# Kernel optimization log

Hardware: AMD Instinct MI355X
Metric: run time of the kernel (lower is better)

Reference implementation:

```python
import jax, jax.numpy as jnp
import numpy as np

D_INPUT = 2048
DD_DIM = 512
DD_PAIRS = DD_DIM // 2


def setup_inputs() -> dict:
    key = jax.random.key(0)
    k1, k2, k3 = jax.random.split(key, 3)
    x = jax.random.normal(k1, (4, 4096, D_INPUT), dtype=jnp.float32)
    # Learned projection (zeros at init in torch; use small random for a non-trivial test)
    W = jax.random.normal(k2, (DD_PAIRS, D_INPUT), dtype=jnp.float32) * 0.02
    b = jax.random.normal(k3, (DD_PAIRS,), dtype=jnp.float32) * 0.02
    return {"x": x, "W": W, "b": b}


def reference(x, W, b):
    # x: (B, T, D); W: (P, D); b: (P,) with P = DD_DIM // 2
    deltas = jnp.einsum('btd,pd->btp', x, W) + b          # (B, T, P)
    angles = jnp.cumsum(deltas, axis=1)                   # cumulative phase
    cos, sin = jnp.cos(angles), jnp.sin(angles)
    x1 = x[..., :DD_PAIRS]                                # (B, T, P)
    x2 = x[..., DD_PAIRS:DD_DIM]                          # (B, T, P)
    rotated = jnp.concatenate([x1 * cos - x2 * sin, x2 * cos + x1 * sin], axis=-1)
    return jnp.concatenate([rotated, x[..., DD_DIM:]], axis=-1)
```

## Files before the change

### kernel.cpp

```cpp
#include <hip/hip_runtime.h>
#include <math.h>

#define BB 4
#define TT 4096
#define DDIM 2048
#define PP 256
#define MM (BB*TT)
#define KKDIM 2048
#define CHUNK 32
#define NCHUNK (TT/CHUNK)

#define BK 64
#define KSTEPS (KKDIM/BK)
#define LSTRA 72

typedef __attribute__((ext_vector_type(8))) short short8;
typedef __attribute__((ext_vector_type(4))) float f32x4;

__device__ __forceinline__ unsigned short f2bf(float f) {
    unsigned u = __float_as_uint(f);
    u += 0x7FFF + ((u >> 16) & 1);
    return (unsigned short)(u >> 16);
}
__device__ __forceinline__ float bf2f(unsigned short h) {
    return __uint_as_float(((unsigned)h) << 16);
}

__device__ __forceinline__ void cvt8(const float4& va, const float4& vb,
                                     short8& hi, short8& lo) {
    float f[8] = {va.x, va.y, va.z, va.w, vb.x, vb.y, vb.z, vb.w};
    #pragma unroll
    for (int j = 0; j < 8; ++j) {
        unsigned short h = f2bf(f[j]);
        hi[j] = (short)h;
        lo[j] = (short)f2bf(f[j] - bf2f(h));
    }
}

__device__ __forceinline__ void cvt4(const float4& v, uint2& hp, uint2& lp) {
    unsigned short h0 = f2bf(v.x), h1 = f2bf(v.y), h2 = f2bf(v.z), h3 = f2bf(v.w);
    unsigned short l0 = f2bf(v.x - bf2f(h0)), l1 = f2bf(v.y - bf2f(h1));
    unsigned short l2 = f2bf(v.z - bf2f(h2)), l3 = f2bf(v.w - bf2f(h3));
    hp.x = (unsigned)h0 | ((unsigned)h1 << 16); hp.y = (unsigned)h2 | ((unsigned)h3 << 16);
    lp.x = (unsigned)l0 | ((unsigned)l1 << 16); lp.y = (unsigned)l2 | ((unsigned)l3 << 16);
}

__global__ __launch_bounds__(256) void prep_wf_k(const float* __restrict__ W,
                                                 unsigned short* __restrict__ Wfh,
                                                 unsigned short* __restrict__ Wfl) {
    const int f = blockIdx.x * 256 + threadIdx.x;
    const int lane = f & 63;
    const int nb   = (f >> 6) & 15;
    const int k0i  = f >> 10;
    const int row  = nb * 16 + (lane & 15);
    const int kk   = k0i * 32 + (lane >> 4) * 8;
    const float* src = W + (size_t)row * KKDIM + kk;
    float4 a = *(const float4*)src;
    float4 b = *(const float4*)(src + 4);
    short8 hi, lo;
    cvt8(a, b, hi, lo);
    *(short8*)(Wfh + (size_t)f * 8) = hi;
    *(short8*)(Wfl + (size_t)f * 8) = lo;
}

__global__ __launch_bounds__(256, 2) void gemm3_k(const float* __restrict__ x,
                                                  const unsigned short* __restrict__ Wfh,
                                                  const unsigned short* __restrict__ Wfl,
                                                  const float* __restrict__ bias,
                                                  float* __restrict__ delta,
                                                  float* __restrict__ csum,
                                                  float* __restrict__ out) {
    __shared__ unsigned short Ahi[2][128 * LSTRA];
    __shared__ unsigned short Alo[2][128 * LSTRA];

    const int hw      = blockIdx.y * 4 + blockIdx.x;
    const int logical = (hw & 7) * 64 + (hw >> 3);
    const int nidx    = logical & 3;
    const int midx    = logical >> 2;
    const int n0      = nidx * 64;
    const int m0      = midx * 128;
    const bool docopy = (nidx == 0);

    const int tid  = threadIdx.x;
    const int w    = tid >> 6;
    const int lane = tid & 63;
    const int lm   = lane & 15;
    const int ko   = lane >> 4;

    const int arow = tid >> 4;
    const int ach  = tid & 15;

    const size_t bfbase = ((size_t)(nidx * 4) * 64 + (size_t)lane) * 8;

    f32x4 acc[2][4];
    #pragma unroll
    for (int i = 0; i < 2; ++i)
        #pragma unroll
        for (int j = 0; j < 4; ++j) {
            f32x4 z = {0.f, 0.f, 0.f, 0.f};
            acc[i][j] = z;
        }

    float4 av[8];
    #pragma unroll
    for (int r = 0; r < 8; ++r)
        av[r] = *(const float4*)(x + (size_t)(m0 + r * 16 + arow) * KKDIM + ach * 4);
    #pragma unroll
    for (int r = 0; r < 8; ++r) {
        uint2 hp, lp;
        cvt4(av[r], hp, lp);
        int idx = (r * 16 + arow) * LSTRA + ach * 4;
        *(uint2*)&Ahi[0][idx] = hp;
        *(uint2*)&Alo[0][idx] = lp;
    }
    short8 bh0[4], bl0[4], bh1[4], bl1[4];
    #pragma unroll
    for (int nt = 0; nt < 4; ++nt) {
        bh0[nt] = *(const short8*)(Wfh + bfbase + (size_t)nt * 512);
        bl0[nt] = *(const short8*)(Wfl + bfbase + (size_t)nt * 512);
    }
    __syncthreads();

    for (int it = 0; it < KSTEPS; ++it) {
        const int  cur  = it & 1, nxt = cur ^ 1;
        const bool last = (it == KSTEPS - 1);
        const int  kA   = last ? it * BK : (it + 1) * BK;

        #pragma unroll
        for (int r = 0; r < 8; ++r)
            av[r] = *(const float4*)(x + (size_t)(m0 + r * 16 + arow) * KKDIM + kA + ach * 4);

        #pragma unroll
        for (int nt = 0; nt < 4; ++nt) {
            size_t o = bfbase + (size_t)((2 * it + 1) * 16 + nt) * 512;
            bh1[nt] = *(const short8*)(Wfh + o);
            bl1[nt] = *(const short8*)(Wfl + o);
        }

        short8 ah[2], al[2];
        #pragma unroll
        for (int mt = 0; mt < 2; ++mt) {
            int idx = (w * 32 + mt * 16 + lm) * LSTRA + ko * 8;
            ah[mt] = *(const short8*)&Ahi[cur][idx];
            al[mt] = *(const short8*)&Alo[cur][idx];
        }
        #pragma unroll
        for (int mt = 0; mt < 2; ++mt)
            #pragma unroll
            for (int nt = 0; nt < 4; ++nt) {
                f32x4 c = acc[mt][nt];
                c = __builtin_amdgcn_mfma_f32_16x16x32_bf16(ah[mt], bh0[nt], c, 0, 0, 0);
                c = __builtin_amdgcn_mfma_f32_16x16x32_bf16(ah[mt], bl0[nt], c, 0, 0, 0);
                c = __builtin_amdgcn_mfma_f32_16x16x32_bf16(al[mt], bh0[nt], c, 0, 0, 0);
                acc[mt][nt] = c;
            }

        const int k0iN = last ? 2 * it : 2 * it + 2;
        #pragma unroll
        for (int nt = 0; nt < 4; ++nt) {
            size_t o = bfbase + (size_t)(k0iN * 16 + nt) * 512;
            bh0[nt] = *(const short8*)(Wfh + o);
            bl0[nt] = *(const short8*)(Wfl + o);
        }

        #pragma unroll
        for (int mt = 0; mt < 2; ++mt) {
            int idx = (w * 32 + mt * 16 + lm) * LSTRA + 32 + ko * 8;
            ah[mt] = *(const short8*)&Ahi[cur][idx];
            al[mt] = *(const short8*)&Alo[cur][idx];
        }
        #pragma unroll
        for (int mt = 0; mt < 2; ++mt)
            #pragma unroll
            for (int nt = 0; nt < 4; ++nt) {
                f32x4 c = acc[mt][nt];
                c = __builtin_amdgcn_mfma_f32_16x16x32_bf16(ah[mt], bh1[nt], c, 0, 0, 0);
                c = __builtin_amdgcn_mfma_f32_16x16x32_bf16(ah[mt], bl1[nt], c, 0, 0, 0);
                c = __builtin_amdgcn_mfma_f32_16x16x32_bf16(al[mt], bh1[nt], c, 0, 0, 0);
                acc[mt][nt] = c;
            }

        #pragma unroll
        for (int r = 0; r < 8; ++r) {
            uint2 hp, lp;
            cvt4(av[r], hp, lp);
            int idx = (r * 16 + arow) * LSTRA + ach * 4;
            *(uint2*)&Ahi[nxt][idx] = hp;
            *(uint2*)&Alo[nxt][idx] = lp;
        }
        if (docopy && !last && kA >= 512) {
            #pragma unroll
            for (int r = 0; r < 8; ++r)
                *(float4*)(out + (size_t)(m0 + r * 16 + arow) * DDIM + kA + ach * 4) = av[r];
        }
        __syncthreads();
    }

    float bsv[4];
    #pragma unroll
    for (int nt = 0; nt < 4; ++nt) bsv[nt] = bias[n0 + nt * 16 + lm];

    float cs[4] = {0.f, 0.f, 0.f, 0.f};
    #pragma unroll
    for (int mt = 0; mt < 2; ++mt)
        #pragma unroll
        for (int nt = 0; nt < 4; ++nt)
            #pragma unroll
            for (int r = 0; r < 4; ++r) {
                float val = acc[mt][nt][r] + bsv[nt];
                int m = m0 + w * 32 + mt * 16 + ko * 4 + r;
                delta[(size_t)m * PP + n0 + nt * 16 + lm] = val;
                cs[nt] += val;
            }
    #pragma unroll
    for (int nt = 0; nt < 4; ++nt) {
        float s = cs[nt];
        s += __shfl_xor(s, 16);
        s += __shfl_xor(s, 32);
        if (lane < 16)
            csum[(size_t)(m0 / CHUNK + w) * PP + n0 + nt * 16 + lane] = s;
    }
}

__global__ __launch_bounds__(256) void rotate2_k(const float* __restrict__ delta,
                                                 const float* __restrict__ csum,
                                                 const float* __restrict__ x,
                                                 float* __restrict__ out) {
    const int bc = blockIdx.x;
    const int c  = bc & (NCHUNK - 1);
    const int b  = bc >> 7;
    const int p  = threadIdx.x;

    const float* cs = csum + (size_t)(b * NCHUNK) * PP + p;
    float angle = 0.f;
    int c0 = 0;
    for (; c0 + 16 <= c; c0 += 16) {
        float v[16];
        #pragma unroll
        for (int j = 0; j < 16; ++j) v[j] = cs[(size_t)(c0 + j) * PP];
        #pragma unroll
        for (int j = 0; j < 16; ++j) angle += v[j];
    }
    for (; c0 < c; ++c0) angle += cs[(size_t)c0 * PP];

    const int tbase = bc * CHUNK;
    const float* dp = delta + (size_t)tbase * PP + p;
    const float* xp = x + (size_t)tbase * DDIM + p;
    float*       op = out + (size_t)tbase * DDIM + p;
    const float inv2pi = 0.15915494309189535f;

    for (int t0 = 0; t0 < CHUNK; t0 += 4) {
        float dv[4], x1v[4], x2v[4];
        #pragma unroll
        for (int j = 0; j < 4; ++j) {
            dv[j]  = dp[(size_t)(t0 + j) * PP];
            x1v[j] = xp[(size_t)(t0 + j) * DDIM];
            x2v[j] = xp[(size_t)(t0 + j) * DDIM + PP];
        }
        #pragma unroll
        for (int j = 0; j < 4; ++j) {
            angle += dv[j];
            float r  = __builtin_amdgcn_fractf(angle * inv2pi);
            float s  = __builtin_amdgcn_sinf(r);
            float co = __builtin_amdgcn_cosf(r);
            op[(size_t)(t0 + j) * DDIM]      = x1v[j] * co - x2v[j] * s;
            op[(size_t)(t0 + j) * DDIM + PP] = x2v[j] * co + x1v[j] * s;
        }
    }
}

__global__ __launch_bounds__(256) void gemm_k(const float* __restrict__ x,
                                              const float* __restrict__ W,
                                              const float* __restrict__ bias,
                                              float* __restrict__ delta,
                                              int dstride, int doff) {
    __shared__ float As[16][68];
    __shared__ float Bs[16][68];
    const int m0  = blockIdx.x * 64;
    const int n0  = blockIdx.y * 64;
    const int tid = threadIdx.x;
    const int lr  = tid >> 2;
    const int lc  = (tid & 3) << 2;
    const int tmi = tid & 15;
    const int tni = tid >> 4;
    float acc[4][4] = {};
    for (int k0 = 0; k0 < KKDIM; k0 += 16) {
        float4 a4 = *(const float4*)(x + (size_t)(m0 + lr) * KKDIM + k0 + lc);
        float4 b4 = *(const float4*)(W + (size_t)(n0 + lr) * KKDIM + k0 + lc);
        __syncthreads();
        As[lc + 0][lr] = a4.x; As[lc + 1][lr] = a4.y;
        As[lc + 2][lr] = a4.z; As[lc + 3][lr] = a4.w;
        Bs[lc + 0][lr] = b4.x; Bs[lc + 1][lr] = b4.y;
        Bs[lc + 2][lr] = b4.z; Bs[lc + 3][lr] = b4.w;
        __syncthreads();
        #pragma unroll
        for (int kk = 0; kk < 16; ++kk) {
            float4 av = *(const float4*)&As[kk][tmi * 4];
            float4 bv = *(const float4*)&Bs[kk][tni * 4];
            float am[4] = {av.x, av.y, av.z, av.w};
            float bn[4] = {bv.x, bv.y, bv.z, bv.w};
            #pragma unroll
            for (int i = 0; i < 4; ++i)
                #pragma unroll
                for (int j = 0; j < 4; ++j)
                    acc[i][j] += am[i] * bn[j];
        }
    }
    const float4 b4 = *(const float4*)(bias + n0 + tni * 4);
    #pragma unroll
    for (int i = 0; i < 4; ++i) {
        size_t m = (size_t)(m0 + tmi * 4 + i);
        float4 o;
        o.x = acc[i][0] + b4.x; o.y = acc[i][1] + b4.y;
        o.z = acc[i][2] + b4.z; o.w = acc[i][3] + b4.w;
        *(float4*)(delta + m * dstride + doff + n0 + tni * 4) = o;
    }
}

__global__ __launch_bounds__(256) void chunksum_k(const float* __restrict__ delta,
                                                  int dstride, int doff,
                                                  float* __restrict__ csum, int cstride) {
    const int bc = blockIdx.x;
    const int b  = bc / NCHUNK;
    const int c  = bc % NCHUNK;
    const int p  = threadIdx.x;
    const int tbase = b * TT + c * CHUNK;
    float s = 0.f;
    #pragma unroll 8
    for (int t = 0; t < CHUNK; ++t)
        s += delta[(size_t)(tbase + t) * dstride + doff + p];
    csum[(size_t)bc * cstride + p] = s;
}

__global__ __launch_bounds__(256) void scan_k(float* __restrict__ csum, int cstride) {
    const int idx = blockIdx.x * 256 + threadIdx.x;
    const int b = idx >> 8;
    const int p = idx & 255;
    float run = 0.f;
    for (int c0 = 0; c0 < NCHUNK; c0 += 8) {
        float v[8];
        #pragma unroll
        for (int j = 0; j < 8; ++j)
            v[j] = csum[(size_t)(b * NCHUNK + c0 + j) * cstride + p];
        #pragma unroll
        for (int j = 0; j < 8; ++j) {
            float t = v[j];
            csum[(size_t)(b * NCHUNK + c0 + j) * cstride + p] = run;
            run += t;
        }
    }
}

__global__ __launch_bounds__(256) void rotate_k(const float* __restrict__ delta,
                                                int dstride, int doff,
                                                const float* __restrict__ csum, int cstride,
                                                const float* __restrict__ x,
                                                float* __restrict__ out) {
    const int bc = blockIdx.x;
    const int p  = threadIdx.x;
    const int tbase = bc * CHUNK;
    float angle = csum[(size_t)bc * cstride + p];
    for (int t = 0; t < CHUNK; ++t) {
        size_t row = (size_t)(tbase + t);
        angle += delta[row * dstride + doff + p];
        float s, co;
        sincosf(angle, &s, &co);
        float x1 = x[row * DDIM + p];
        float x2 = x[row * DDIM + PP + p];
        out[row * DDIM + p]      = x1 * co - x2 * s;
        out[row * DDIM + PP + p] = x2 * co + x1 * s;
    }
}

__global__ __launch_bounds__(256) void copy_k(const float* __restrict__ x,
                                              float* __restrict__ out) {
    const size_t row = (size_t)blockIdx.x * 4 + (threadIdx.x >> 6);
    const int lane = threadIdx.x & 63;
    const int col = 512 + (blockIdx.y * 64 + lane) * 4;
    const size_t a = row * DDIM + col;
    *(float4*)(out + a) = *(const float4*)(x + a);
}

extern "C" void kernel_launch(void* const* d_in, const int* in_sizes, int n_in,
                              void* d_out, int out_size, void* d_ws, size_t ws_size,
                              hipStream_t stream) {
    const float* x    = (const float*)d_in[0];
    const float* W    = (const float*)d_in[1];
    const float* bias = (const float*)d_in[2];
    float* out = (float*)d_out;

    const size_t delta_elems = (size_t)MM * PP;
    const size_t csum_elems  = (size_t)BB * NCHUNK * PP;
    const size_t w_elems     = (size_t)PP * KKDIM;
    const size_t need = (delta_elems + csum_elems) * sizeof(float)
                      + 2 * w_elems * sizeof(unsigned short);

    if (ws_size >= need) {
        float* delta = (float*)d_ws;
        float* csum  = (float*)d_ws + delta_elems;
        unsigned short* Wfh = (unsigned short*)(csum + csum_elems);
        unsigned short* Wfl = Wfh + w_elems;
        prep_wf_k<<<256, 256, 0, stream>>>(W, Wfh, Wfl);
        gemm3_k<<<dim3(4, MM / 128), 256, 0, stream>>>(x, Wfh, Wfl, bias,
                                                       delta, csum, out);
        rotate2_k<<<BB * NCHUNK, 256, 0, stream>>>(delta, csum, x, out);
    } else {
        float* delta = out; const int dstride = DDIM, doff = 512;
        float* csum  = out + 768; const int cstride = DDIM;
        gemm_k<<<dim3(MM / 64, PP / 64), 256, 0, stream>>>(x, W, bias, delta, dstride, doff);
        chunksum_k<<<BB * NCHUNK, 256, 0, stream>>>(delta, dstride, doff, csum, cstride);
        scan_k<<<(BB * PP) / 256, 256, 0, stream>>>(csum, cstride);
        rotate_k<<<BB * NCHUNK, 256, 0, stream>>>(delta, dstride, doff, csum, cstride, x, out);
        copy_k<<<dim3(MM / 4, 6), 256, 0, stream>>>(x, out);
    }
}
```

Measured before the change: 327.8 us.

## Split GEMM over 8 waves with smaller K-step and split rotate into segments

The GEMM kernel now runs 512 threads per block, with waves split 4x2 over M and N. Each wave computes a 32x32 tile instead of 32x64, and the K step drops to 32 with the hi/lo bf16 planes interleaved in a single shared buffer. The rotate kernel launches four blocks per chunk, each handling 8 timesteps after recomputing the partial prefix from delta. This aims to raise occupancy and parallelism and to shorten the serial per-chunk work. The cost is twice as many barriers per K and redundant prefix reads of delta in the rotate kernel.

```diff
diff --git a/kernel.cpp b/kernel.cpp
--- a/kernel.cpp
+++ b/kernel.cpp
@@ -10,9 +10,9 @@
 #define CHUNK 32
 #define NCHUNK (TT/CHUNK)
 
-#define BK 64
+#define BK 32
 #define KSTEPS (KKDIM/BK)
-#define LSTRA 72
+#define LROW 72
 
 typedef __attribute__((ext_vector_type(8))) short short8;
 typedef __attribute__((ext_vector_type(4))) float f32x4;
@@ -63,15 +63,58 @@
     *(short8*)(Wfl + (size_t)f * 8) = lo;
 }
 
-__global__ __launch_bounds__(256, 2) void gemm3_k(const float* __restrict__ x,
+#define GSTEP(CUR, NXT, BHc, BLc, BHn, BLn, IT)                               \
+{                                                                             \
+    const bool last_ = ((IT) == KSTEPS - 1);                                  \
+    const int  kA_   = last_ ? (IT) * BK : ((IT) + 1) * BK;                   \
+    float4 av0_ = *(const float4*)(xs0 + kA_);                                \
+    float4 av1_ = *(const float4*)(xs1 + kA_);                                \
+    const int k0iN_ = last_ ? (IT) : (IT) + 1;                                \
+    _Pragma("unroll")                                                         \
+    for (int nt = 0; nt < 2; ++nt) {                                          \
+        size_t o = bfbase + (size_t)(k0iN_ * 16 + nt) * 512;                  \
+        BHn[nt] = *(const short8*)(Wfh + o);                                  \
+        BLn[nt] = *(const short8*)(Wfl + o);                                  \
+    }                                                                         \
+    short8 ah_[2], al_[2];                                                    \
+    _Pragma("unroll")                                                         \
+    for (int mt = 0; mt < 2; ++mt) {                                          \
+        int idx = (wm * 32 + mt * 16 + lm) * LROW + ko * 8;                   \
+        ah_[mt] = *(const short8*)&Ast[CUR][idx];                             \
+        al_[mt] = *(const short8*)&Ast[CUR][idx + 32];                        \
+    }                                                                         \
+    _Pragma("unroll")                                                         \
+    for (int mt = 0; mt < 2; ++mt)                                            \
+        _Pragma("unroll")                                                     \
+        for (int nt = 0; nt < 2; ++nt) {                                      \
+            f32x4 c = acc[mt][nt];                                            \
+            c = __builtin_amdgcn_mfma_f32_16x16x32_bf16(ah_[mt], BHc[nt], c, 0, 0, 0); \
+            c = __builtin_amdgcn_mfma_f32_16x16x32_bf16(ah_[mt], BLc[nt], c, 0, 0, 0); \
+            c = __builtin_amdgcn_mfma_f32_16x16x32_bf16(al_[mt], BHc[nt], c, 0, 0, 0); \
+            acc[mt][nt] = c;                                                  \
+        }                                                                     \
+    uint2 hp0_, lp0_, hp1_, lp1_;                                             \
+    cvt4(av0_, hp0_, lp0_);                                                   \
+    cvt4(av1_, hp1_, lp1_);                                                   \
+    *(uint2*)&Ast[NXT][sidx0]      = hp0_;                                    \
+    *(uint2*)&Ast[NXT][sidx0 + 32] = lp0_;                                    \
+    *(uint2*)&Ast[NXT][sidx1]      = hp1_;                                    \
+    *(uint2*)&Ast[NXT][sidx1 + 32] = lp1_;                                    \
+    if (docopy && !last_ && kA_ >= 512) {                                     \
+        *(float4*)(os0 + kA_) = av0_;                                         \
+        *(float4*)(os1 + kA_) = av1_;                                         \
+    }                                                                         \
+    __syncthreads();                                                          \
+}
+
+__global__ __launch_bounds__(512, 4) void gemm4_k(const float* __restrict__ x,
                                                   const unsigned short* __restrict__ Wfh,
                                                   const unsigned short* __restrict__ Wfl,
                                                   const float* __restrict__ bias,
                                                   float* __restrict__ delta,
                                                   float* __restrict__ csum,
                                                   float* __restrict__ out) {
-    __shared__ unsigned short Ahi[2][128 * LSTRA];
-    __shared__ unsigned short Alo[2][128 * LSTRA];
+    __shared__ unsigned short Ast[2][128 * LROW];
 
     const int hw      = blockIdx.y * 4 + blockIdx.x;
     const int logical = (hw & 7) * 64 + (hw >> 3);
@@ -83,153 +126,94 @@
 
     const int tid  = threadIdx.x;
     const int w    = tid >> 6;
+    const int wm   = w >> 1;
+    const int wn   = w & 1;
     const int lane = tid & 63;
     const int lm   = lane & 15;
     const int ko   = lane >> 4;
 
-    const int arow = tid >> 4;
-    const int ach  = tid & 15;
-
-    const size_t bfbase = ((size_t)(nidx * 4) * 64 + (size_t)lane) * 8;
-
-    f32x4 acc[2][4];
+    const int arow0 = tid >> 3;
+    const int ach   = tid & 7;
+    const int sidx0 = arow0 * LROW + ach * 4;
+    const int sidx1 = (64 + arow0) * LROW + ach * 4;
+    const float* xs0 = x + (size_t)(m0 + arow0) * KKDIM + ach * 4;
+    const float* xs1 = x + (size_t)(m0 + 64 + arow0) * KKDIM + ach * 4;
+    float* os0 = out + (size_t)(m0 + arow0) * DDIM + ach * 4;
+    float* os1 = out + (size_t)(m0 + 64 + arow0) * DDIM + ach * 4;
+
+    const size_t bfbase = ((size_t)(nidx * 4 + wn * 2) * 64 + (size_t)lane) * 8;
+
+    f32x4 acc[2][2];
     #pragma unroll
     for (int i = 0; i < 2; ++i)
         #pragma unroll
-        for (int j = 0; j < 4; ++j) {
+        for (int j = 0; j < 2; ++j) {
             f32x4 z = {0.f, 0.f, 0.f, 0.f};
             acc[i][j] = z;
         }
 
-    float4 av[8];
-    #pragma unroll
-    for (int r = 0; r < 8; ++r)
-        av[r] = *(const float4*)(x + (size_t)(m0 + r * 16 + arow) * KKDIM + ach * 4);
-    #pragma unroll
-    for (int r = 0; r < 8; ++r) {
+    short8 bhA[2], blA[2], bhB[2], blB[2];
+
+    {
+        float4 a0 = *(const float4*)(xs0);
+        float4 a1 = *(const float4*)(xs1);
         uint2 hp, lp;
-        cvt4(av[r], hp, lp);
-        int idx = (r * 16 + arow) * LSTRA + ach * 4;
-        *(uint2*)&Ahi[0][idx] = hp;
-        *(uint2*)&Alo[0][idx] = lp;
-    }
-    short8 bh0[4], bl0[4], bh1[4], bl1[4];
-    #pragma unroll
-    for (int nt = 0; nt < 4; ++nt) {
-        bh0[nt] = *(const short8*)(Wfh + bfbase + (size_t)nt * 512);
-        bl0[nt] = *(const short8*)(Wfl + bfbase + (size_t)nt * 512);
-    }
-    __syncthreads();
-
-    for (int it = 0; it < KSTEPS; ++it) {
-        const int  cur  = it & 1, nxt = cur ^ 1;
-        const bool last = (it == KSTEPS - 1);
-        const int  kA   = last ? it * BK : (it + 1) * BK;
-
-        #pragma unroll
-        for (int r = 0; r < 8; ++r)
-            av[r] = *(const float4*)(x + (size_t)(m0 + r * 16 + arow) * KKDIM + kA + ach * 4);
-
-        #pragma unroll
-        for (int nt = 0; nt < 4; ++nt) {
-            size_t o = bfbase + (size_t)((2 * it + 1) * 16 + nt) * 512;
-            bh1[nt] = *(const short8*)(Wfh + o);
-            bl1[nt] = *(const short8*)(Wfl + o);
-        }
-
-        short8 ah[2], al[2];
-        #pragma unroll
-        for (int mt = 0; mt < 2; ++mt) {
-            int idx = (w * 32 + mt * 16 + lm) * LSTRA + ko * 8;
-            ah[mt] = *(const short8*)&Ahi[cur][idx];
-            al[mt] = *(const short8*)&Alo[cur][idx];
-        }
-        #pragma unroll
-        for (int mt = 0; mt < 2; ++mt)
-            #pragma unroll
-            for (int nt = 0; nt < 4; ++nt) {
-                f32x4 c = acc[mt][nt];
-                c = __builtin_amdgcn_mfma_f32_16x16x32_bf16(ah[mt], bh0[nt], c, 0, 0, 0);
-                c = __builtin_amdgcn_mfma_f32_16x16x32_bf16(ah[mt], bl0[nt], c, 0, 0, 0);
-                c = __builtin_amdgcn_mfma_f32_16x16x32_bf16(al[mt], bh0[nt], c, 0, 0, 0);
-                acc[mt][nt] = c;
-            }
-
-        const int k0iN = last ? 2 * it : 2 * it + 2;
-        #pragma unroll
-        for (int nt = 0; nt < 4; ++nt) {
-            size_t o = bfbase + (size_t)(k0iN * 16 + nt) * 512;
-            bh0[nt] = *(const short8*)(Wfh + o);
-            bl0[nt] = *(const short8*)(Wfl + o);
-        }
-
-        #pragma unroll
-        for (int mt = 0; mt < 2; ++mt) {
-            int idx = (w * 32 + mt * 16 + lm) * LSTRA + 32 + ko * 8;
-            ah[mt] = *(const short8*)&Ahi[cur][idx];
-            al[mt] = *(const short8*)&Alo[cur][idx];
-        }
-        #pragma unroll
-        for (int mt = 0; mt < 2; ++mt)
-            #pragma unroll
-            for (int nt = 0; nt < 4; ++nt) {
-                f32x4 c = acc[mt][nt];
-                c = __builtin_amdgcn_mfma_f32_16x16x32_bf16(ah[mt], bh1[nt], c, 0, 0, 0);
-                c = __builtin_amdgcn_mfma_f32_16x16x32_bf16(ah[mt], bl1[nt], c, 0, 0, 0);
-                c = __builtin_amdgcn_mfma_f32_16x16x32_bf16(al[mt], bh1[nt], c, 0, 0, 0);
-                acc[mt][nt] = c;
-            }
-
-        #pragma unroll
-        for (int r = 0; r < 8; ++r) {
-            uint2 hp, lp;
-            cvt4(av[r], hp, lp);
-            int idx = (r * 16 + arow) * LSTRA + ach * 4;
-            *(uint2*)&Ahi[nxt][idx] = hp;
-            *(uint2*)&Alo[nxt][idx] = lp;
-        }
-        if (docopy && !last && kA >= 512) {
-            #pragma unroll
-            for (int r = 0; r < 8; ++r)
-                *(float4*)(out + (size_t)(m0 + r * 16 + arow) * DDIM + kA + ach * 4) = av[r];
+        cvt4(a0, hp, lp);
+        *(uint2*)&Ast[0][sidx0]      = hp;
+        *(uint2*)&Ast[0][sidx0 + 32] = lp;
+        cvt4(a1, hp, lp);
+        *(uint2*)&Ast[0][sidx1]      = hp;
+        *(uint2*)&Ast[0][sidx1 + 32] = lp;
+        #pragma unroll
+        for (int nt = 0; nt < 2; ++nt) {
+            size_t o = bfbase + (size_t)nt * 512;
+            bhA[nt] = *(const short8*)(Wfh + o);
+            blA[nt] = *(const short8*)(Wfl + o);
         }
         __syncthreads();
     }
 
-    float bsv[4];
-    #pragma unroll
-    for (int nt = 0; nt < 4; ++nt) bsv[nt] = bias[n0 + nt * 16 + lm];
-
-    float cs[4] = {0.f, 0.f, 0.f, 0.f};
+    for (int it = 0; it < KSTEPS; it += 2) {
+        GSTEP(0, 1, bhA, blA, bhB, blB, it)
+        GSTEP(1, 0, bhB, blB, bhA, blA, it + 1)
+    }
+
+    float bsv[2];
+    #pragma unroll
+    for (int nt = 0; nt < 2; ++nt) bsv[nt] = bias[n0 + wn * 32 + nt * 16 + lm];
+
+    float cs[2] = {0.f, 0.f};
     #pragma unroll
     for (int mt = 0; mt < 2; ++mt)
         #pragma unroll
-        for (int nt = 0; nt < 4; ++nt)
+        for (int nt = 0; nt < 2; ++nt)
             #pragma unroll
             for (int r = 0; r < 4; ++r) {
                 float val = acc[mt][nt][r] + bsv[nt];
-                int m = m0 + w * 32 + mt * 16 + ko * 4 + r;
-                delta[(size_t)m * PP + n0 + nt * 16 + lm] = val;
+                int m = m0 + wm * 32 + mt * 16 + ko * 4 + r;
+                delta[(size_t)m * PP + n0 + wn * 32 + nt * 16 + lm] = val;
                 cs[nt] += val;
             }
     #pragma unroll
-    for (int nt = 0; nt < 4; ++nt) {
+    for (int nt = 0; nt < 2; ++nt) {
         float s = cs[nt];
         s += __shfl_xor(s, 16);
         s += __shfl_xor(s, 32);
         if (lane < 16)
-            csum[(size_t)(m0 / CHUNK + w) * PP + n0 + nt * 16 + lane] = s;
-    }
-}
-
-__global__ __launch_bounds__(256) void rotate2_k(const float* __restrict__ delta,
+            csum[(size_t)(m0 / CHUNK + wm) * PP + n0 + wn * 32 + nt * 16 + lane] = s;
+    }
+}
+
+__global__ __launch_bounds__(256) void rotate4_k(const float* __restrict__ delta,
                                                  const float* __restrict__ csum,
                                                  const float* __restrict__ x,
                                                  float* __restrict__ out) {
-    const int bc = blockIdx.x;
-    const int c  = bc & (NCHUNK - 1);
-    const int b  = bc >> 7;
-    const int p  = threadIdx.x;
+    const int blk = blockIdx.x;
+    const int seg = blk & 3;
+    const int bc  = blk >> 2;
+    const int c   = bc & (NCHUNK - 1);
+    const int b   = bc >> 7;
+    const int p   = threadIdx.x;
 
     const float* cs = csum + (size_t)(b * NCHUNK) * PP + p;
     float angle = 0.f;
@@ -245,11 +229,21 @@
 
     const int tbase = bc * CHUNK;
     const float* dp = delta + (size_t)tbase * PP + p;
+
+    const int tpre = seg * 8;
+    for (int t = 0; t < tpre; t += 8) {
+        float v[8];
+        #pragma unroll
+        for (int j = 0; j < 8; ++j) v[j] = dp[(size_t)(t + j) * PP];
+        #pragma unroll
+        for (int j = 0; j < 8; ++j) angle += v[j];
+    }
+
     const float* xp = x + (size_t)tbase * DDIM + p;
     float*       op = out + (size_t)tbase * DDIM + p;
     const float inv2pi = 0.15915494309189535f;
 
-    for (int t0 = 0; t0 < CHUNK; t0 += 4) {
+    for (int t0 = tpre; t0 < tpre + 8; t0 += 4) {
         float dv[4], x1v[4], x2v[4];
         #pragma unroll
         for (int j = 0; j < 4; ++j) {
@@ -401,9 +395,9 @@
         unsigned short* Wfh = (unsigned short*)(csum + csum_elems);
         unsigned short* Wfl = Wfh + w_elems;
         prep_wf_k<<<256, 256, 0, stream>>>(W, Wfh, Wfl);
-        gemm3_k<<<dim3(4, MM / 128), 256, 0, stream>>>(x, Wfh, Wfl, bias,
+        gemm4_k<<<dim3(4, MM / 128), 512, 0, stream>>>(x, Wfh, Wfl, bias,
                                                        delta, csum, out);
-        rotate2_k<<<BB * NCHUNK, 256, 0, stream>>>(delta, csum, x, out);
+        rotate4_k<<<BB * NCHUNK * 4, 256, 0, stream>>>(delta, csum, x, out);
     } else {
         float* delta = out; const int dstride = DDIM, doff = 512;
         float* csum  = out + 768; const int cstride = DDIM;
```

Measured after the change: 316.1 us. -3.6%, faster.
